# Kernel tuning notes

Hardware: AMD Instinct MI355X
Metric: run time of the kernel (lower is better)

## Reference

```python
import jax, jax.numpy as jnp
import numpy as np

B, NQ, C, H, P, DFF = 4, 2500, 256, 8, 8, 512
BEV_H, BEV_W = 200, 200
DH = C // H


def _ln(x, g, b, eps=1e-5):
    m = x.mean(-1, keepdims=True)
    v = ((x - m) ** 2).mean(-1, keepdims=True)
    return (x - m) / jnp.sqrt(v + eps) * g + b


def setup_inputs() -> dict:
    key = jax.random.key(0)
    ks = jax.random.split(key, 16)
    s = 0.02
    f32 = jnp.float32
    return {
        'query': jax.random.normal(ks[0], (B, NQ, C), f32),
        'value': jax.random.normal(ks[1], (B, BEV_H * BEV_W, C), f32),
        'query_pos': jax.random.normal(ks[2], (B, NQ, C), f32),
        'ref_2d': jax.random.uniform(ks[3], (B, NQ, 1, 2), f32),
        'in_proj_w': jax.random.normal(ks[4], (3 * C, C), f32) * s,
        'in_proj_b': jnp.zeros((3 * C,), f32),
        'out_proj_w': jax.random.normal(ks[5], (C, C), f32) * s,
        'out_proj_b': jnp.zeros((C,), f32),
        'off_w': jax.random.normal(ks[6], (H * P * 2, C), f32) * s,
        'off_b': jax.random.normal(ks[7], (H * P * 2,), f32),
        'aw_w': jax.random.normal(ks[8], (H * P, C), f32) * s,
        'aw_b': jnp.zeros((H * P,), f32),
        'vproj_w': jax.random.normal(ks[9], (C, C), f32) * s,
        'vproj_b': jnp.zeros((C,), f32),
        'oproj_w': jax.random.normal(ks[10], (C, C), f32) * s,
        'oproj_b': jnp.zeros((C,), f32),
        'ffn_w1': jax.random.normal(ks[11], (DFF, C), f32) * s,
        'ffn_b1': jnp.zeros((DFF,), f32),
        'ffn_w2': jax.random.normal(ks[12], (C, DFF), f32) * s,
        'ffn_b2': jnp.zeros((C,), f32),
        'ln1_g': jnp.ones((C,), f32), 'ln1_b': jnp.zeros((C,), f32),
        'ln2_g': jnp.ones((C,), f32), 'ln2_b': jnp.zeros((C,), f32),
        'ln3_g': jnp.ones((C,), f32), 'ln3_b': jnp.zeros((C,), f32),
        'bev_h': BEV_H,
        'bev_w': BEV_W,
    }


def _deform_attn(q, val_flat, ref, off_w, off_b, aw_w, aw_b,
                 vproj_w, vproj_b, oproj_w, oproj_b, bev_h, bev_w):
    # MSDeformAttn with n_levels=1 (Deformable-DETR math, align_corners=False bilinear).
    Bq, Nq, Cq = q.shape
    val = (val_flat @ vproj_w.T + vproj_b).reshape(Bq, bev_h * bev_w, H, DH)
    off = (q @ off_w.T + off_b).reshape(Bq, Nq, H, P, 2)
    aw = jax.nn.softmax((q @ aw_w.T + aw_b).reshape(Bq, Nq, H, P), axis=-1)
    norm = jnp.array([bev_w, bev_h], jnp.float32)  # offsets normalized by (W, H)
    # ref: (B, Nq, 1, 2) broadcasts over heads/points -> (B, Nq, H, P, 2)
    loc = ref[:, :, None, :, :] + off / norm
    # grid_sample(align_corners=False): pixel = loc * size - 0.5
    x = loc[..., 0] * bev_w - 0.5
    y = loc[..., 1] * bev_h - 0.5
    x0 = jnp.floor(x)
    y0 = jnp.floor(y)
    lx = x - x0
    ly = y - y0
    x0i = x0.astype(jnp.int32)
    y0i = y0.astype(jnp.int32)
    b_idx = jnp.arange(Bq)[:, None, None, None]
    h_idx = jnp.arange(H)[None, None, :, None]

    def gather(yi, xi):
        valid = (xi >= 0) & (xi < bev_w) & (yi >= 0) & (yi < bev_h)
        idx = jnp.clip(yi, 0, bev_h - 1) * bev_w + jnp.clip(xi, 0, bev_w - 1)
        g = val[b_idx, idx, h_idx]  # (B, Nq, H, P, DH)
        return g * valid[..., None]

    w00 = ((1 - lx) * (1 - ly))[..., None]
    w01 = (lx * (1 - ly))[..., None]
    w10 = ((1 - lx) * ly)[..., None]
    w11 = (lx * ly)[..., None]
    samp = (gather(y0i, x0i) * w00 + gather(y0i, x0i + 1) * w01
            + gather(y0i + 1, x0i) * w10 + gather(y0i + 1, x0i + 1) * w11)
    out = (samp * aw[..., None]).sum(axis=3).reshape(Bq, Nq, Cq)
    return out @ oproj_w.T + oproj_b


def _forward(query, value, query_pos, ref_2d,
             in_proj_w, in_proj_b, out_proj_w, out_proj_b,
             off_w, off_b, aw_w, aw_b, vproj_w, vproj_b, oproj_w, oproj_b,
             ffn_w1, ffn_b1, ffn_w2, ffn_b2,
             ln1_g, ln1_b, ln2_g, ln2_b, ln3_g, ln3_b, bev_h, bev_w):
    Bq, Nq, Cq = query.shape
    # ---- self attention (q = query + pos, k = v = query) ----
    Wq, Wk, Wv = in_proj_w[:C], in_proj_w[C:2 * C], in_proj_w[2 * C:]
    bq, bk, bv = in_proj_b[:C], in_proj_b[C:2 * C], in_proj_b[2 * C:]
    q = ((query + query_pos) @ Wq.T + bq).reshape(Bq, Nq, H, DH)
    k = (query @ Wk.T + bk).reshape(Bq, Nq, H, DH)
    v = (query @ Wv.T + bv).reshape(Bq, Nq, H, DH)
    scores = jnp.einsum('bqhd,bkhd->bhqk', q, k) / jnp.sqrt(jnp.float32(DH))
    attn = jax.nn.softmax(scores, axis=-1)
    sa = jnp.einsum('bhqk,bkhd->bqhd', attn, v).reshape(Bq, Nq, Cq)
    sa = sa @ out_proj_w.T + out_proj_b
    x = sa + query
    identity = x
    x = _ln(x, ln1_g, ln1_b)
    # ---- deformable cross attention ----
    ca = _deform_attn(x, value, ref_2d, off_w, off_b, aw_w, aw_b,
                      vproj_w, vproj_b, oproj_w, oproj_b, bev_h, bev_w)
    x = ca + identity
    x = _ln(x, ln2_g, ln2_b)
    # ---- FFN with internal residual ----
    x = x + (jax.nn.relu(x @ ffn_w1.T + ffn_b1) @ ffn_w2.T + ffn_b2)
    x = _ln(x, ln3_g, ln3_b)
    return x


def reference(query, value, query_pos, ref_2d,
              in_proj_w, in_proj_b, out_proj_w, out_proj_b,
              off_w, off_b, aw_w, aw_b, vproj_w, vproj_b, oproj_w, oproj_b,
              ffn_w1, ffn_b1, ffn_w2, ffn_b2,
              ln1_g, ln1_b, ln2_g, ln2_b, ln3_g, ln3_b, bev_h, bev_w):
    return _forward(query, value, query_pos, ref_2d,
                    in_proj_w, in_proj_b, out_proj_w, out_proj_b,
                    off_w, off_b, aw_w, aw_b, vproj_w, vproj_b, oproj_w, oproj_b,
                    ffn_w1, ffn_b1, ffn_w2, ffn_b2,
                    ln1_g, ln1_b, ln2_g, ln2_b, ln3_g, ln3_b, bev_h, bev_w)
```

## Files before the change

kernel.cpp:

```cpp
#include <hip/hip_runtime.h>

#define BB   4
#define NQ   2500
#define CC   256
#define HH   8
#define PP   8
#define DFFN 512
#define DH   32
#define BEV  200
#define NVAL (BEV * BEV)

typedef short bf16x8 __attribute__((ext_vector_type(8)));
typedef float f32x4  __attribute__((ext_vector_type(4)));

__device__ __forceinline__ unsigned short f2b(float f) {
    union { float f; unsigned int u; } v; v.f = f;
    unsigned int r = v.u + 0x7fffu + ((v.u >> 16) & 1u);
    return (unsigned short)(r >> 16);
}
__device__ __forceinline__ float b2f(unsigned short b) {
    union { unsigned int u; float f; } v; v.u = ((unsigned int)b) << 16;
    return v.f;
}

#define GLOAD16(g, l)                                                         \
    __builtin_amdgcn_global_load_lds(                                         \
        (const __attribute__((address_space(1))) void*)(g),                   \
        (__attribute__((address_space(3))) void*)(l), 16, 0, 0)

__global__ __launch_bounds__(256) void add_cvt_qp(const float* __restrict__ q,
                                                  const float* __restrict__ p,
                                                  unsigned short* __restrict__ qpb,
                                                  unsigned short* __restrict__ qb,
                                                  int n4) {
    int i = blockIdx.x * 256 + threadIdx.x;
    if (i < n4) {
        float4 a = reinterpret_cast<const float4*>(q)[i];
        float4 b = reinterpret_cast<const float4*>(p)[i];
        ushort4 s, t;
        s.x = f2b(a.x); s.y = f2b(a.y); s.z = f2b(a.z); s.w = f2b(a.w);
        t.x = f2b(a.x + b.x); t.y = f2b(a.y + b.y);
        t.z = f2b(a.z + b.z); t.w = f2b(a.w + b.w);
        reinterpret_cast<ushort4*>(qb)[i]  = s;
        reinterpret_cast<ushort4*>(qpb)[i] = t;
    }
}

__global__ __launch_bounds__(256) void cvt4(const float* __restrict__ in,
                                            unsigned short* __restrict__ out, int n4) {
    int i = blockIdx.x * 256 + threadIdx.x;
    if (i < n4) {
        float4 a = reinterpret_cast<const float4*>(in)[i];
        ushort4 s;
        s.x = f2b(a.x); s.y = f2b(a.y); s.z = f2b(a.z); s.w = f2b(a.w);
        reinterpret_cast<ushort4*>(out)[i] = s;
    }
}

__global__ __launch_bounds__(256) void cvt_weights(const float* __restrict__ in_w,
                                                   const float* __restrict__ outp_w,
                                                   const float* __restrict__ vproj_w,
                                                   const float* __restrict__ oproj_w,
                                                   const float* __restrict__ ffn_w1,
                                                   const float* __restrict__ ffn_w2,
                                                   unsigned short* __restrict__ Wb) {
    int i = blockIdx.x * 256 + threadIdx.x;
    if (i >= 163840) return;
    const float* src; int base;
    if      (i <  49152) { src = in_w;    base = 0;      }
    else if (i <  65536) { src = outp_w;  base = 49152;  }
    else if (i <  81920) { src = vproj_w; base = 65536;  }
    else if (i <  98304) { src = oproj_w; base = 81920;  }
    else if (i < 131072) { src = ffn_w1;  base = 98304;  }
    else                 { src = ffn_w2;  base = 131072; }
    float4 a = reinterpret_cast<const float4*>(src)[i - base];
    ushort4 s;
    s.x = f2b(a.x); s.y = f2b(a.y); s.z = f2b(a.z); s.w = f2b(a.w);
    reinterpret_cast<ushort4*>(Wb)[i] = s;
}

#define TM 128
#define TN 128
#define TK 32
template <bool RELU, bool OBF>
__global__ __launch_bounds__(256) void gemm_mfma(const unsigned short* __restrict__ A,
                                                 const unsigned short* __restrict__ W,
                                                 const float* __restrict__ bias,
                                                 float* __restrict__ Cf,
                                                 unsigned short* __restrict__ Cb,
                                                 int M, int N, int K) {
    __shared__ __align__(16) unsigned short As[TM * TK];
    __shared__ __align__(16) unsigned short Ws[TN * TK];
    const int t    = threadIdx.x;
    const int lane = t & 63;
    const int wv   = t >> 6;
    const int wr   = wv >> 1;
    const int wc   = wv & 1;
    const int m0 = blockIdx.y * TM;
    const int n0 = blockIdx.x * TN;
    const int l15 = lane & 15;
    const int l4  = lane >> 4;

    const int srow = (lane >> 2);
    const int skk  = (lane & 3) << 3;

    f32x4 acc[4][4];
#pragma unroll
    for (int i = 0; i < 4; i++)
#pragma unroll
        for (int j = 0; j < 4; j++) acc[i][j] = (f32x4){0.f, 0.f, 0.f, 0.f};

    for (int k0 = 0; k0 < K; k0 += TK) {
#pragma unroll
        for (int c2 = 0; c2 < 2; c2++) {
            const int c = wv * 2 + c2;
            const int row = c * 16 + srow;
            int ar = m0 + row; if (ar >= M) ar = M - 1;
            int br = n0 + row; if (br >= N) br = N - 1;
            GLOAD16(A + (size_t)ar * K + k0 + skk, As + c * 512);
            GLOAD16(W + (size_t)br * K + k0 + skk, Ws + c * 512);
        }
        __syncthreads();

        bf16x8 af[4], bfr[4];
#pragma unroll
        for (int i = 0; i < 4; i++) {
            af[i]  = *reinterpret_cast<const bf16x8*>(&As[(wr * 64 + i * 16 + l15) * TK + l4 * 8]);
            bfr[i] = *reinterpret_cast<const bf16x8*>(&Ws[(wc * 64 + i * 16 + l15) * TK + l4 * 8]);
        }
#pragma unroll
        for (int i = 0; i < 4; i++)
#pragma unroll
            for (int j = 0; j < 4; j++)
                acc[i][j] = __builtin_amdgcn_mfma_f32_16x16x32_bf16(af[i], bfr[j], acc[i][j], 0, 0, 0);
        __syncthreads();
    }

#pragma unroll
    for (int i = 0; i < 4; i++) {
#pragma unroll
        for (int j = 0; j < 4; j++) {
            const int col = n0 + wc * 64 + j * 16 + l15;
            const float bv = bias[col];
#pragma unroll
            for (int r = 0; r < 4; r++) {
                const int row = m0 + wr * 64 + i * 16 + l4 * 4 + r;
                if (row < M) {
                    float v = acc[i][j][r] + bv;
                    if (RELU) v = fmaxf(v, 0.f);
                    if (OBF) Cb[(size_t)row * N + col] = f2b(v);
                    else     Cf[(size_t)row * N + col] = v;
                }
            }
        }
    }
}

#define BM 64
#define BN 64
#define BK 16
__global__ __launch_bounds__(256) void gemm_bias(const float* __restrict__ A,
                                                 const float* __restrict__ W,
                                                 const float* __restrict__ bias,
                                                 float* __restrict__ C,
                                                 int M, int N, int K) {
    __shared__ float As[BK][BM + 4];
    __shared__ float Ws[BK][BN + 4];
    const int m0 = blockIdx.y * BM;
    const int n0 = blockIdx.x * BN;
    const int t  = threadIdx.x;
    const int tx = t & 15;
    const int ty = t >> 4;
    const int lrow = t >> 2;
    const int lk   = (t & 3) << 2;

    float acc[4][4];
#pragma unroll
    for (int i = 0; i < 4; i++)
#pragma unroll
        for (int j = 0; j < 4; j++) acc[i][j] = 0.f;

    const bool aok = (m0 + lrow) < M;
    const float* Ap = A + (size_t)(m0 + lrow) * K + lk;
    const float* Wp = W + (size_t)(n0 + lrow) * K + lk;

    for (int k0 = 0; k0 < K; k0 += BK) {
        float4 av = make_float4(0.f, 0.f, 0.f, 0.f);
        if (aok) av = *reinterpret_cast<const float4*>(Ap + k0);
        float4 wv = *reinterpret_cast<const float4*>(Wp + k0);
        As[lk + 0][lrow] = av.x; As[lk + 1][lrow] = av.y;
        As[lk + 2][lrow] = av.z; As[lk + 3][lrow] = av.w;
        Ws[lk + 0][lrow] = wv.x; Ws[lk + 1][lrow] = wv.y;
        Ws[lk + 2][lrow] = wv.z; Ws[lk + 3][lrow] = wv.w;
        __syncthreads();
#pragma unroll
        for (int kk = 0; kk < BK; kk++) {
            float4 a4 = *reinterpret_cast<const float4*>(&As[kk][ty << 2]);
            float4 w4 = *reinterpret_cast<const float4*>(&Ws[kk][tx << 2]);
            float a[4] = {a4.x, a4.y, a4.z, a4.w};
            float w[4] = {w4.x, w4.y, w4.z, w4.w};
#pragma unroll
            for (int i = 0; i < 4; i++)
#pragma unroll
                for (int j = 0; j < 4; j++)
                    acc[i][j] = fmaf(a[i], w[j], acc[i][j]);
        }
        __syncthreads();
    }

    float4 b4 = *reinterpret_cast<const float4*>(bias + n0 + (tx << 2));
#pragma unroll
    for (int i = 0; i < 4; i++) {
        int row = m0 + (ty << 2) + i;
        if (row < M) {
            float4 o;
            o.x = acc[i][0] + b4.x; o.y = acc[i][1] + b4.y;
            o.z = acc[i][2] + b4.z; o.w = acc[i][3] + b4.w;
            *reinterpret_cast<float4*>(C + (size_t)row * N + n0 + (tx << 2)) = o;
        }
    }
}

#define QT 64
#define KTT 64
#define NTQ ((NQ + QT - 1) / QT)
#define NTK ((NQ + KTT - 1) / KTT)
#define VLD (KTT + 8)

__global__ __launch_bounds__(256) void flash_mfma(const unsigned short* __restrict__ Q,
                                                  const unsigned short* __restrict__ K,
                                                  const unsigned short* __restrict__ V,
                                                  unsigned short* __restrict__ O) {
    __shared__ __align__(16) unsigned short VT[2][DH][VLD];
    __shared__ __align__(16) unsigned short PL[4][16][VLD];

    const int bh = blockIdx.y;
    const int b = bh >> 3, h = bh & 7;
    const int t = threadIdx.x;
    const int w = t >> 6;
    const int lane = t & 63;
    const int l15 = lane & 15;
    const int g = lane >> 4;
    const int q0 = blockIdx.x * QT;
    const float scale = 0.17677669529663687f;

    const size_t kvb = (size_t)b * NQ * CC + h * DH;

    int qr = q0 + w * 16 + l15; if (qr >= NQ) qr = NQ - 1;
    const bf16x8 qfrag = *reinterpret_cast<const bf16x8*>(Q + kvb + (size_t)qr * CC + g * 8);

    const int skey = t >> 2;
    const int sd0  = (t & 3) << 3;

    {
        int kr = skey; if (kr >= NQ) kr = NQ - 1;
        bf16x8 vv = *reinterpret_cast<const bf16x8*>(V + kvb + (size_t)kr * CC + sd0);
#pragma unroll
        for (int j2 = 0; j2 < 8; j2++) VT[0][sd0 + j2][skey] = (unsigned short)vv[j2];
    }
    bf16x8 kf[4];
#pragma unroll
    for (int j = 0; j < 4; j++) {
        int kr = j * 16 + l15; if (kr >= NQ) kr = NQ - 1;
        kf[j] = *reinterpret_cast<const bf16x8*>(K + kvb + (size_t)kr * CC + g * 8);
    }
    __syncthreads();

    float m = -1e30f, l = 0.f;
    f32x4 o0 = {0.f, 0.f, 0.f, 0.f}, o1 = {0.f, 0.f, 0.f, 0.f};

    for (int kt = 0; kt < NTK; kt++) {
        const int cur = kt & 1;

        if (kt + 1 < NTK) {
            int kr = (kt + 1) * KTT + skey; if (kr >= NQ) kr = NQ - 1;
            bf16x8 vv = *reinterpret_cast<const bf16x8*>(V + kvb + (size_t)kr * CC + sd0);
#pragma unroll
            for (int j2 = 0; j2 < 8; j2++) VT[cur ^ 1][sd0 + j2][skey] = (unsigned short)vv[j2];
        }

        f32x4 sf[4];
#pragma unroll
        for (int j = 0; j < 4; j++)
            sf[j] = __builtin_amdgcn_mfma_f32_16x16x32_bf16(kf[j], qfrag,
                                                            (f32x4){0.f, 0.f, 0.f, 0.f}, 0, 0, 0);

        if (kt + 1 < NTK) {
#pragma unroll
            for (int j = 0; j < 4; j++) {
                int kr = (kt + 1) * KTT + j * 16 + l15; if (kr >= NQ) kr = NQ - 1;
                kf[j] = *reinterpret_cast<const bf16x8*>(K + kvb + (size_t)kr * CC + g * 8);
            }
        }

        float sv[16];
#pragma unroll
        for (int j = 0; j < 4; j++)
#pragma unroll
            for (int r = 0; r < 4; r++) {
                int key = kt * KTT + j * 16 + g * 4 + r;
                sv[j * 4 + r] = (key < NQ) ? sf[j][r] * scale : -1e30f;
            }

        float mx = sv[0];
#pragma unroll
        for (int i = 1; i < 16; i++) mx = fmaxf(mx, sv[i]);
        mx = fmaxf(mx, __shfl_xor(mx, 16));
        mx = fmaxf(mx, __shfl_xor(mx, 32));
        float mn = fmaxf(m, mx);
        float cor = __expf(m - mn);
        m = mn;

        float ps = 0.f;
#pragma unroll
        for (int j = 0; j < 4; j++) {
            ushort4 pk;
            float p0 = __expf(sv[j * 4 + 0] - mn);
            float p1 = __expf(sv[j * 4 + 1] - mn);
            float p2 = __expf(sv[j * 4 + 2] - mn);
            float p3 = __expf(sv[j * 4 + 3] - mn);
            ps += (p0 + p1) + (p2 + p3);
            pk.x = f2b(p0); pk.y = f2b(p1); pk.z = f2b(p2); pk.w = f2b(p3);
            *reinterpret_cast<ushort4*>(&PL[w][l15][j * 16 + g * 4]) = pk;
        }
        ps += __shfl_xor(ps, 16);
        ps += __shfl_xor(ps, 32);
        l = l * cor + ps;
        o0 *= cor; o1 *= cor;

#pragma unroll
        for (int ks = 0; ks < 2; ks++) {
            bf16x8 pf = *reinterpret_cast<const bf16x8*>(&PL[w][l15][ks * 32 + g * 8]);
            bf16x8 va = *reinterpret_cast<const bf16x8*>(&VT[cur][l15][ks * 32 + g * 8]);
            bf16x8 vc = *reinterpret_cast<const bf16x8*>(&VT[cur][16 + l15][ks * 32 + g * 8]);
            o0 = __builtin_amdgcn_mfma_f32_16x16x32_bf16(va, pf, o0, 0, 0, 0);
            o1 = __builtin_amdgcn_mfma_f32_16x16x32_bf16(vc, pf, o1, 0, 0, 0);
        }

        __syncthreads();
    }

    int q = q0 + w * 16 + l15;
    if (q < NQ) {
        float inv = 1.f / l;
        unsigned short* op = O + ((size_t)b * NQ + q) * CC + h * DH;
#pragma unroll
        for (int r = 0; r < 4; r++) {
            op[g * 4 + r]      = f2b(o0[r] * inv);
            op[16 + g * 4 + r] = f2b(o1[r] * inv);
        }
    }
}

__global__ __launch_bounds__(256) void resid_ln(const float* __restrict__ a,
                                                const float* __restrict__ r,
                                                const float* __restrict__ g,
                                                const float* __restrict__ be,
                                                float* __restrict__ sum_out,
                                                float* __restrict__ ln_out,
                                                unsigned short* __restrict__ ln_bf) {
    const int row = blockIdx.x;
    const int t = threadIdx.x;
    const size_t base = (size_t)row * CC;
    float v = a[base + t] + r[base + t];
    if (sum_out) sum_out[base + t] = v;

    __shared__ float red[4];
    float s = v;
#pragma unroll
    for (int o = 1; o < 64; o <<= 1) s += __shfl_xor(s, o, 64);
    if ((t & 63) == 0) red[t >> 6] = s;
    __syncthreads();
    float mean = (red[0] + red[1] + red[2] + red[3]) * (1.f / 256.f);
    __syncthreads();

    float d = v - mean;
    float sq = d * d;
#pragma unroll
    for (int o = 1; o < 64; o <<= 1) sq += __shfl_xor(sq, o, 64);
    if ((t & 63) == 0) red[t >> 6] = sq;
    __syncthreads();
    float var = (red[0] + red[1] + red[2] + red[3]) * (1.f / 256.f);

    float res = d * rsqrtf(var + 1e-5f) * g[t] + be[t];
    ln_out[base + t] = res;
    if (ln_bf) ln_bf[base + t] = f2b(res);
}

__global__ __launch_bounds__(256) void deform_sample(const unsigned short* __restrict__ val,
                                                     const float* __restrict__ off,
                                                     const float* __restrict__ awl,
                                                     const float* __restrict__ ref,
                                                     unsigned short* __restrict__ out) {
    const int bq = blockIdx.x;
    const int b = bq / NQ;
    const int t = threadIdx.x;
    const int h = t >> 5, d = t & 31;

    const float rx = ref[(size_t)bq * 2 + 0];
    const float ry = ref[(size_t)bq * 2 + 1];

    const float* ap = awl + (size_t)bq * (HH * PP) + h * PP;
    float aw[PP];
    float mx = -1e30f;
#pragma unroll
    for (int p = 0; p < PP; p++) { aw[p] = ap[p]; mx = fmaxf(mx, aw[p]); }
    float se = 0.f;
#pragma unroll
    for (int p = 0; p < PP; p++) { aw[p] = __expf(aw[p] - mx); se += aw[p]; }
    const float inv = 1.f / se;

    const float* op = off + (size_t)bq * (HH * PP * 2) + h * (PP * 2);
    const unsigned short* vb = val + (size_t)b * NVAL * CC + h * DH + d;

    float acc = 0.f;
#pragma unroll
    for (int p = 0; p < PP; p++) {
        float x = (rx + op[p * 2 + 0] * (1.f / BEV)) * (float)BEV - 0.5f;
        float y = (ry + op[p * 2 + 1] * (1.f / BEV)) * (float)BEV - 0.5f;
        float xf = floorf(x), yf = floorf(y);
        float lx = x - xf, ly = y - yf;
        int x0 = (int)xf, y0 = (int)yf;
        float w = aw[p] * inv;

        float s = 0.f;
#pragma unroll
        for (int c = 0; c < 4; c++) {
            int xi = x0 + (c & 1);
            int yi = y0 + (c >> 1);
            float wx = (c & 1) ? lx : (1.f - lx);
            float wy = (c >> 1) ? ly : (1.f - ly);
            bool vld = (xi >= 0) && (xi < BEV) && (yi >= 0) && (yi < BEV);
            int xc = min(max(xi, 0), BEV - 1);
            int yc = min(max(yi, 0), BEV - 1);
            float gv = b2f(vb[(size_t)(yc * BEV + xc) * CC]);
            s += vld ? (wx * wy * gv) : 0.f;
        }
        acc = fmaf(w, s, acc);
    }
    out[(size_t)bq * CC + t] = f2b(acc);
}

extern "C" void kernel_launch(void* const* d_in, const int* in_sizes, int n_in,
                              void* d_out, int out_size, void* d_ws, size_t ws_size,
                              hipStream_t stream) {
    const float* query   = (const float*)d_in[0];
    const float* value   = (const float*)d_in[1];
    const float* qpos    = (const float*)d_in[2];
    const float* ref2d   = (const float*)d_in[3];
    const float* in_w    = (const float*)d_in[4];
    const float* in_b    = (const float*)d_in[5];
    const float* outp_w  = (const float*)d_in[6];
    const float* outp_b  = (const float*)d_in[7];
    const float* off_w   = (const float*)d_in[8];
    const float* off_b   = (const float*)d_in[9];
    const float* aw_w    = (const float*)d_in[10];
    const float* aw_b    = (const float*)d_in[11];
    const float* vproj_w = (const float*)d_in[12];
    const float* vproj_b = (const float*)d_in[13];
    const float* oproj_w = (const float*)d_in[14];
    const float* oproj_b = (const float*)d_in[15];
    const float* ffn_w1  = (const float*)d_in[16];
    const float* ffn_b1  = (const float*)d_in[17];
    const float* ffn_w2  = (const float*)d_in[18];
    const float* ffn_b2  = (const float*)d_in[19];
    const float* ln1_g = (const float*)d_in[20], *ln1_b = (const float*)d_in[21];
    const float* ln2_g = (const float*)d_in[22], *ln2_b = (const float*)d_in[23];
    const float* ln3_g = (const float*)d_in[24], *ln3_b = (const float*)d_in[25];

    float* ws = (float*)d_ws;
    float* out = (float*)d_out;

    const int M = BB * NQ;

    unsigned short* QPb    = (unsigned short*)ws;
    unsigned short* QUERYb = (unsigned short*)(ws + 1280000);
    unsigned short* Qbb    = (unsigned short*)(ws + 2560000);
    unsigned short* Kbb    = (unsigned short*)(ws + 3840000);
    unsigned short* Vbb    = (unsigned short*)(ws + 5120000);
    unsigned short* ATTb   = (unsigned short*)(ws + 6400000);
    float* SA   = ws + 7680000;
    unsigned short* VALUEb = (unsigned short*)ws;
    unsigned short* VALb = (unsigned short*)(ws + 20480000);
    float* B3   = ws + 40960000;
    float* X1   = B3;
    float* XLN1 = B3 + 2560000;
    float* OFF  = B3 + 5120000;
    float* AWL  = B3 + 6400000;
    unsigned short* SAMPb = (unsigned short*)(B3 + 7040000);
    float* CA   = B3 + 8320000;
    float* XLN2 = B3 + 10880000;
    unsigned short* XLN2b = (unsigned short*)(B3 + 13440000);
    unsigned short* FFNHb = (unsigned short*)(B3 + 14720000);
    float* FFNO = B3 + 17280000;
    unsigned short* Wb = (unsigned short*)(B3 + 19840000);

    dim3 blk(256);
    const int mgT = (M + TM - 1) / TM;

    add_cvt_qp<<<dim3(2500), blk, 0, stream>>>(query, qpos, QPb, QUERYb, 640000);
    cvt_weights<<<dim3(640), blk, 0, stream>>>(in_w, outp_w, vproj_w, oproj_w, ffn_w1, ffn_w2, Wb);
    gemm_mfma<false, true><<<dim3(2, mgT), blk, 0, stream>>>(QPb,    Wb,          in_b,        nullptr, Qbb, M, CC, CC);
    gemm_mfma<false, true><<<dim3(2, mgT), blk, 0, stream>>>(QUERYb, Wb + 65536,  in_b + CC,   nullptr, Kbb, M, CC, CC);
    gemm_mfma<false, true><<<dim3(2, mgT), blk, 0, stream>>>(QUERYb, Wb + 131072, in_b + 2*CC, nullptr, Vbb, M, CC, CC);
    flash_mfma<<<dim3(NTQ, BB * HH), blk, 0, stream>>>(Qbb, Kbb, Vbb, ATTb);
    gemm_mfma<false, false><<<dim3(2, mgT), blk, 0, stream>>>(ATTb, Wb + 196608, outp_b, SA, nullptr, M, CC, CC);
    resid_ln<<<dim3(M), blk, 0, stream>>>(SA, query, ln1_g, ln1_b, X1, XLN1, nullptr);
    gemm_bias<<<dim3(2, (M + BM - 1) / BM), blk, 0, stream>>>(XLN1, off_w, off_b, OFF, M, 128, CC);
    gemm_bias<<<dim3(1, (M + BM - 1) / BM), blk, 0, stream>>>(XLN1, aw_w,  aw_b,  AWL, M, 64,  CC);
    cvt4<<<dim3(40000), blk, 0, stream>>>(value, VALUEb, 10240000);
    gemm_mfma<false, true><<<dim3(2, (BB * NVAL) / TM), blk, 0, stream>>>(VALUEb, Wb + 262144, vproj_b, nullptr, VALb, BB * NVAL, CC, CC);
    deform_sample<<<dim3(M), blk, 0, stream>>>(VALb, OFF, AWL, ref2d, SAMPb);
    gemm_mfma<false, false><<<dim3(2, mgT), blk, 0, stream>>>(SAMPb, Wb + 327680, oproj_b, CA, nullptr, M, CC, CC);
    resid_ln<<<dim3(M), blk, 0, stream>>>(CA, X1, ln2_g, ln2_b, nullptr, XLN2, XLN2b);
    gemm_mfma<true,  true ><<<dim3(4, mgT), blk, 0, stream>>>(XLN2b, Wb + 393216, ffn_b1, nullptr, FFNHb, M, DFFN, CC);
    gemm_mfma<false, false><<<dim3(2, mgT), blk, 0, stream>>>(FFNHb, Wb + 524288, ffn_b2, FFNO, nullptr, M, CC, DFFN);
    resid_ln<<<dim3(M), blk, 0, stream>>>(FFNO, XLN2, ln3_g, ln3_b, nullptr, out, nullptr);
}
```

Baseline: 680.9 us.

## Fuse value conversion into vproj GEMM, split flash attention, merge K/V and off/aw GEMMs

Several independent changes land together. The separate fp32→bf16 conversion of the large value tensor is folded into a new vproj MFMA GEMM that converts while loading its A tile. The K and V projections become a single N=512 GEMM. Flash attention is split into two key chunks with a combine kernel, doubling grid parallelism. The fp32 SIMT offset and attention-weight GEMMs become one bf16 MFMA GEMM fed by a bf16 LN output. These remove a large intermediate round trip and some launches, at the cost of extra partial-result traffic for the attention split and bf16 rounding in the offset projection.

After: 639.0 us. -6.1%, faster.

```diff
diff --git a/kernel.cpp b/kernel.cpp
--- a/kernel.cpp
+++ b/kernel.cpp
@@ -11,6 +11,7 @@
 #define NVAL (BEV * BEV)
 
 typedef short bf16x8 __attribute__((ext_vector_type(8)));
+typedef unsigned short u16x8 __attribute__((ext_vector_type(8)));
 typedef float f32x4  __attribute__((ext_vector_type(4)));
 
 __device__ __forceinline__ unsigned short f2b(float f) {
@@ -46,33 +47,26 @@
     }
 }
 
-__global__ __launch_bounds__(256) void cvt4(const float* __restrict__ in,
-                                            unsigned short* __restrict__ out, int n4) {
-    int i = blockIdx.x * 256 + threadIdx.x;
-    if (i < n4) {
-        float4 a = reinterpret_cast<const float4*>(in)[i];
-        ushort4 s;
-        s.x = f2b(a.x); s.y = f2b(a.y); s.z = f2b(a.z); s.w = f2b(a.w);
-        reinterpret_cast<ushort4*>(out)[i] = s;
-    }
-}
-
 __global__ __launch_bounds__(256) void cvt_weights(const float* __restrict__ in_w,
                                                    const float* __restrict__ outp_w,
                                                    const float* __restrict__ vproj_w,
                                                    const float* __restrict__ oproj_w,
                                                    const float* __restrict__ ffn_w1,
                                                    const float* __restrict__ ffn_w2,
+                                                   const float* __restrict__ off_w,
+                                                   const float* __restrict__ aw_w,
                                                    unsigned short* __restrict__ Wb) {
     int i = blockIdx.x * 256 + threadIdx.x;
-    if (i >= 163840) return;
+    if (i >= 176128) return;
     const float* src; int base;
     if      (i <  49152) { src = in_w;    base = 0;      }
     else if (i <  65536) { src = outp_w;  base = 49152;  }
     else if (i <  81920) { src = vproj_w; base = 65536;  }
     else if (i <  98304) { src = oproj_w; base = 81920;  }
     else if (i < 131072) { src = ffn_w1;  base = 98304;  }
-    else                 { src = ffn_w2;  base = 131072; }
+    else if (i < 163840) { src = ffn_w2;  base = 131072; }
+    else if (i < 172032) { src = off_w;   base = 163840; }
+    else                 { src = aw_w;    base = 172032; }
     float4 a = reinterpret_cast<const float4*>(src)[i - base];
     ushort4 s;
     s.x = f2b(a.x); s.y = f2b(a.y); s.z = f2b(a.z); s.w = f2b(a.w);
@@ -156,67 +150,157 @@
     }
 }
 
-#define BM 64
-#define BN 64
-#define BK 16
-__global__ __launch_bounds__(256) void gemm_bias(const float* __restrict__ A,
-                                                 const float* __restrict__ W,
-                                                 const float* __restrict__ bias,
-                                                 float* __restrict__ C,
-                                                 int M, int N, int K) {
-    __shared__ float As[BK][BM + 4];
-    __shared__ float Ws[BK][BN + 4];
-    const int m0 = blockIdx.y * BM;
-    const int n0 = blockIdx.x * BN;
-    const int t  = threadIdx.x;
-    const int tx = t & 15;
-    const int ty = t >> 4;
-    const int lrow = t >> 2;
-    const int lk   = (t & 3) << 2;
-
-    float acc[4][4];
+#define VP_LDA 40
+__global__ __launch_bounds__(256) void gemm_vproj(const float* __restrict__ A,
+                                                  const unsigned short* __restrict__ W,
+                                                  const float* __restrict__ bias,
+                                                  unsigned short* __restrict__ Cb,
+                                                  int M, int N, int K) {
+    __shared__ __align__(16) unsigned short As[TM * VP_LDA];
+    __shared__ __align__(16) unsigned short Ws[TN * TK];
+    const int t    = threadIdx.x;
+    const int lane = t & 63;
+    const int wv   = t >> 6;
+    const int wr   = wv >> 1;
+    const int wc   = wv & 1;
+    const int m0 = blockIdx.y * TM;
+    const int n0 = blockIdx.x * TN;
+    const int l15 = lane & 15;
+    const int l4  = lane >> 4;
+    const int srow = (lane >> 2);
+    const int skk  = (lane & 3) << 3;
+    const int arow = t & 127;
+    const int akh  = t >> 7;
+
+    f32x4 acc[4][4];
 #pragma unroll
     for (int i = 0; i < 4; i++)
 #pragma unroll
-        for (int j = 0; j < 4; j++) acc[i][j] = 0.f;
-
-    const bool aok = (m0 + lrow) < M;
-    const float* Ap = A + (size_t)(m0 + lrow) * K + lk;
-    const float* Wp = W + (size_t)(n0 + lrow) * K + lk;
-
-    for (int k0 = 0; k0 < K; k0 += BK) {
-        float4 av = make_float4(0.f, 0.f, 0.f, 0.f);
-        if (aok) av = *reinterpret_cast<const float4*>(Ap + k0);
-        float4 wv = *reinterpret_cast<const float4*>(Wp + k0);
-        As[lk + 0][lrow] = av.x; As[lk + 1][lrow] = av.y;
-        As[lk + 2][lrow] = av.z; As[lk + 3][lrow] = av.w;
-        Ws[lk + 0][lrow] = wv.x; Ws[lk + 1][lrow] = wv.y;
-        Ws[lk + 2][lrow] = wv.z; Ws[lk + 3][lrow] = wv.w;
+        for (int j = 0; j < 4; j++) acc[i][j] = (f32x4){0.f, 0.f, 0.f, 0.f};
+
+    int ar = m0 + arow; if (ar >= M) ar = M - 1;
+    const float* ap = A + (size_t)ar * K + akh * 16;
+
+    for (int k0 = 0; k0 < K; k0 += TK) {
+#pragma unroll
+        for (int c2 = 0; c2 < 2; c2++) {
+            const int c = wv * 2 + c2;
+            int br = n0 + c * 16 + srow; if (br >= N) br = N - 1;
+            GLOAD16(W + (size_t)br * K + k0 + skk, Ws + c * 512);
+        }
+        float4 f0 = *reinterpret_cast<const float4*>(ap + k0);
+        float4 f1 = *reinterpret_cast<const float4*>(ap + k0 + 4);
+        float4 f2 = *reinterpret_cast<const float4*>(ap + k0 + 8);
+        float4 f3 = *reinterpret_cast<const float4*>(ap + k0 + 12);
+        u16x8 pa, pb;
+        pa[0] = f2b(f0.x); pa[1] = f2b(f0.y); pa[2] = f2b(f0.z); pa[3] = f2b(f0.w);
+        pa[4] = f2b(f1.x); pa[5] = f2b(f1.y); pa[6] = f2b(f1.z); pa[7] = f2b(f1.w);
+        pb[0] = f2b(f2.x); pb[1] = f2b(f2.y); pb[2] = f2b(f2.z); pb[3] = f2b(f2.w);
+        pb[4] = f2b(f3.x); pb[5] = f2b(f3.y); pb[6] = f2b(f3.z); pb[7] = f2b(f3.w);
+        *reinterpret_cast<u16x8*>(&As[arow * VP_LDA + akh * 16])     = pa;
+        *reinterpret_cast<u16x8*>(&As[arow * VP_LDA + akh * 16 + 8]) = pb;
         __syncthreads();
-#pragma unroll
-        for (int kk = 0; kk < BK; kk++) {
-            float4 a4 = *reinterpret_cast<const float4*>(&As[kk][ty << 2]);
-            float4 w4 = *reinterpret_cast<const float4*>(&Ws[kk][tx << 2]);
-            float a[4] = {a4.x, a4.y, a4.z, a4.w};
-            float w[4] = {w4.x, w4.y, w4.z, w4.w};
-#pragma unroll
-            for (int i = 0; i < 4; i++)
-#pragma unroll
-                for (int j = 0; j < 4; j++)
-                    acc[i][j] = fmaf(a[i], w[j], acc[i][j]);
-        }
+
+        bf16x8 af[4], bfr[4];
+#pragma unroll
+        for (int i = 0; i < 4; i++) {
+            af[i]  = *reinterpret_cast<const bf16x8*>(&As[(wr * 64 + i * 16 + l15) * VP_LDA + l4 * 8]);
+            bfr[i] = *reinterpret_cast<const bf16x8*>(&Ws[(wc * 64 + i * 16 + l15) * TK + l4 * 8]);
+        }
+#pragma unroll
+        for (int i = 0; i < 4; i++)
+#pragma unroll
+            for (int j = 0; j < 4; j++)
+                acc[i][j] = __builtin_amdgcn_mfma_f32_16x16x32_bf16(af[i], bfr[j], acc[i][j], 0, 0, 0);
         __syncthreads();
     }
 
-    float4 b4 = *reinterpret_cast<const float4*>(bias + n0 + (tx << 2));
 #pragma unroll
     for (int i = 0; i < 4; i++) {
-        int row = m0 + (ty << 2) + i;
-        if (row < M) {
-            float4 o;
-            o.x = acc[i][0] + b4.x; o.y = acc[i][1] + b4.y;
-            o.z = acc[i][2] + b4.z; o.w = acc[i][3] + b4.w;
-            *reinterpret_cast<float4*>(C + (size_t)row * N + n0 + (tx << 2)) = o;
+#pragma unroll
+        for (int j = 0; j < 4; j++) {
+            const int col = n0 + wc * 64 + j * 16 + l15;
+            const float bv = bias[col];
+#pragma unroll
+            for (int r = 0; r < 4; r++) {
+                const int row = m0 + wr * 64 + i * 16 + l4 * 4 + r;
+                if (row < M)
+                    Cb[(size_t)row * N + col] = f2b(acc[i][j][r] + bv);
+            }
+        }
+    }
+}
+
+__global__ __launch_bounds__(256) void gemm_offaw(const unsigned short* __restrict__ A,
+                                                  const unsigned short* __restrict__ W,
+                                                  const float* __restrict__ off_b,
+                                                  const float* __restrict__ aw_b,
+                                                  float* __restrict__ OFF,
+                                                  float* __restrict__ AWL,
+                                                  int M) {
+    __shared__ __align__(16) unsigned short As[TM * TK];
+    __shared__ __align__(16) unsigned short Ws[64 * TK];
+    const int t    = threadIdx.x;
+    const int lane = t & 63;
+    const int wv   = t >> 6;
+    const int wr   = wv >> 1;
+    const int wc   = wv & 1;
+    const int m0 = blockIdx.y * TM;
+    const int n0 = blockIdx.x * 64;
+    const int l15 = lane & 15;
+    const int l4  = lane >> 4;
+    const int srow = (lane >> 2);
+    const int skk  = (lane & 3) << 3;
+
+    f32x4 acc[4][2];
+#pragma unroll
+    for (int i = 0; i < 4; i++)
+#pragma unroll
+        for (int j = 0; j < 2; j++) acc[i][j] = (f32x4){0.f, 0.f, 0.f, 0.f};
+
+    for (int k0 = 0; k0 < 256; k0 += TK) {
+#pragma unroll
+        for (int c2 = 0; c2 < 2; c2++) {
+            const int c = wv * 2 + c2;
+            int ar = m0 + c * 16 + srow; if (ar >= M) ar = M - 1;
+            GLOAD16(A + (size_t)ar * 256 + k0 + skk, As + c * 512);
+        }
+        {
+            int br = n0 + wv * 16 + srow;
+            GLOAD16(W + (size_t)br * 256 + k0 + skk, Ws + wv * 512);
+        }
+        __syncthreads();
+
+        bf16x8 af[4], bw[2];
+#pragma unroll
+        for (int i = 0; i < 4; i++)
+            af[i] = *reinterpret_cast<const bf16x8*>(&As[(wr * 64 + i * 16 + l15) * TK + l4 * 8]);
+#pragma unroll
+        for (int j = 0; j < 2; j++)
+            bw[j] = *reinterpret_cast<const bf16x8*>(&Ws[(wc * 32 + j * 16 + l15) * TK + l4 * 8]);
+#pragma unroll
+        for (int i = 0; i < 4; i++)
+#pragma unroll
+            for (int j = 0; j < 2; j++)
+                acc[i][j] = __builtin_amdgcn_mfma_f32_16x16x32_bf16(af[i], bw[j], acc[i][j], 0, 0, 0);
+        __syncthreads();
+    }
+
+#pragma unroll
+    for (int i = 0; i < 4; i++) {
+#pragma unroll
+        for (int j = 0; j < 2; j++) {
+            const int gc = n0 + wc * 32 + j * 16 + l15;
+            const float bv = (gc < 128) ? off_b[gc] : aw_b[gc - 128];
+#pragma unroll
+            for (int r = 0; r < 4; r++) {
+                const int row = m0 + wr * 64 + i * 16 + l4 * 4 + r;
+                if (row < M) {
+                    float v = acc[i][j][r] + bv;
+                    if (gc < 128) OFF[(size_t)row * 128 + gc] = v;
+                    else          AWL[(size_t)row * 64 + (gc - 128)] = v;
+                }
+            }
         }
     }
 }
@@ -224,16 +308,18 @@
 #define QT 64
 #define KTT 64
 #define NTQ ((NQ + QT - 1) / QT)
-#define NTK ((NQ + KTT - 1) / KTT)
+#define CHK 1280
+#define NTK2 (CHK / KTT)
 #define VLD (KTT + 8)
 
-__global__ __launch_bounds__(256) void flash_mfma(const unsigned short* __restrict__ Q,
-                                                  const unsigned short* __restrict__ K,
-                                                  const unsigned short* __restrict__ V,
-                                                  unsigned short* __restrict__ O) {
+__global__ __launch_bounds__(256) void flash_part(const unsigned short* __restrict__ Q,
+                                                  const unsigned short* __restrict__ KV,
+                                                  float* __restrict__ PART,
+                                                  float* __restrict__ ML) {
     __shared__ __align__(16) unsigned short VT[2][DH][VLD];
     __shared__ __align__(16) unsigned short PL[4][16][VLD];
 
+    const int c  = blockIdx.z;
     const int bh = blockIdx.y;
     const int b = bh >> 3, h = bh & 7;
     const int t = threadIdx.x;
@@ -242,39 +328,40 @@
     const int l15 = lane & 15;
     const int g = lane >> 4;
     const int q0 = blockIdx.x * QT;
+    const int kc0 = c * CHK;
     const float scale = 0.17677669529663687f;
 
-    const size_t kvb = (size_t)b * NQ * CC + h * DH;
+    const size_t qbase = (size_t)b * NQ;
 
     int qr = q0 + w * 16 + l15; if (qr >= NQ) qr = NQ - 1;
-    const bf16x8 qfrag = *reinterpret_cast<const bf16x8*>(Q + kvb + (size_t)qr * CC + g * 8);
+    const bf16x8 qfrag = *reinterpret_cast<const bf16x8*>(Q + (qbase + qr) * CC + h * DH + g * 8);
 
     const int skey = t >> 2;
     const int sd0  = (t & 3) << 3;
 
     {
-        int kr = skey; if (kr >= NQ) kr = NQ - 1;
-        bf16x8 vv = *reinterpret_cast<const bf16x8*>(V + kvb + (size_t)kr * CC + sd0);
+        int kr = kc0 + skey; if (kr >= NQ) kr = NQ - 1;
+        bf16x8 vv = *reinterpret_cast<const bf16x8*>(KV + (qbase + kr) * 512 + 256 + h * DH + sd0);
 #pragma unroll
         for (int j2 = 0; j2 < 8; j2++) VT[0][sd0 + j2][skey] = (unsigned short)vv[j2];
     }
     bf16x8 kf[4];
 #pragma unroll
     for (int j = 0; j < 4; j++) {
-        int kr = j * 16 + l15; if (kr >= NQ) kr = NQ - 1;
-        kf[j] = *reinterpret_cast<const bf16x8*>(K + kvb + (size_t)kr * CC + g * 8);
+        int kr = kc0 + j * 16 + l15; if (kr >= NQ) kr = NQ - 1;
+        kf[j] = *reinterpret_cast<const bf16x8*>(KV + (qbase + kr) * 512 + h * DH + g * 8);
     }
     __syncthreads();
 
     float m = -1e30f, l = 0.f;
     f32x4 o0 = {0.f, 0.f, 0.f, 0.f}, o1 = {0.f, 0.f, 0.f, 0.f};
 
-    for (int kt = 0; kt < NTK; kt++) {
+    for (int kt = 0; kt < NTK2; kt++) {
         const int cur = kt & 1;
 
-        if (kt + 1 < NTK) {
-            int kr = (kt + 1) * KTT + skey; if (kr >= NQ) kr = NQ - 1;
-            bf16x8 vv = *reinterpret_cast<const bf16x8*>(V + kvb + (size_t)kr * CC + sd0);
+        if (kt + 1 < NTK2) {
+            int kr = kc0 + (kt + 1) * KTT + skey; if (kr >= NQ) kr = NQ - 1;
+            bf16x8 vv = *reinterpret_cast<const bf16x8*>(KV + (qbase + kr) * 512 + 256 + h * DH + sd0);
 #pragma unroll
             for (int j2 = 0; j2 < 8; j2++) VT[cur ^ 1][sd0 + j2][skey] = (unsigned short)vv[j2];
         }
@@ -285,11 +372,11 @@
             sf[j] = __builtin_amdgcn_mfma_f32_16x16x32_bf16(kf[j], qfrag,
                                                             (f32x4){0.f, 0.f, 0.f, 0.f}, 0, 0, 0);
 
-        if (kt + 1 < NTK) {
+        if (kt + 1 < NTK2) {
 #pragma unroll
             for (int j = 0; j < 4; j++) {
-                int kr = (kt + 1) * KTT + j * 16 + l15; if (kr >= NQ) kr = NQ - 1;
-                kf[j] = *reinterpret_cast<const bf16x8*>(K + kvb + (size_t)kr * CC + g * 8);
+                int kr = kc0 + (kt + 1) * KTT + j * 16 + l15; if (kr >= NQ) kr = NQ - 1;
+                kf[j] = *reinterpret_cast<const bf16x8*>(KV + (qbase + kr) * 512 + h * DH + g * 8);
             }
         }
 
@@ -298,7 +385,7 @@
         for (int j = 0; j < 4; j++)
 #pragma unroll
             for (int r = 0; r < 4; r++) {
-                int key = kt * KTT + j * 16 + g * 4 + r;
+                int key = kc0 + kt * KTT + j * 16 + g * 4 + r;
                 sv[j * 4 + r] = (key < NQ) ? sf[j][r] * scale : -1e30f;
             }
 
@@ -342,14 +429,36 @@
 
     int q = q0 + w * 16 + l15;
     if (q < NQ) {
-        float inv = 1.f / l;
-        unsigned short* op = O + ((size_t)b * NQ + q) * CC + h * DH;
-#pragma unroll
-        for (int r = 0; r < 4; r++) {
-            op[g * 4 + r]      = f2b(o0[r] * inv);
-            op[16 + g * 4 + r] = f2b(o1[r] * inv);
-        }
-    }
+        float* pp = PART + ((size_t)(c * (BB * HH) + bh) * NQ + q) * 32;
+        *reinterpret_cast<f32x4*>(pp + g * 4)      = o0;
+        *reinterpret_cast<f32x4*>(pp + 16 + g * 4) = o1;
+        if (g == 0) {
+            float* mp = ML + ((size_t)(c * (BB * HH) + bh) * NQ + q) * 2;
+            mp[0] = m; mp[1] = l;
+        }
+    }
+}
+
+__global__ __launch_bounds__(256) void flash_combine(const float* __restrict__ PART,
+                                                     const float* __restrict__ ML,
+                                                     unsigned short* __restrict__ O) {
+    const int idx = blockIdx.x * 256 + threadIdx.x;
+    const int bq = idx >> 8;
+    const int hd = idx & 255;
+    const int h = hd >> 5, dd = hd & 31;
+    const int b = bq / NQ, q = bq - b * NQ;
+    const int bh = b * HH + h;
+
+    const float* mp0 = ML + ((size_t)bh * NQ + q) * 2;
+    const float* mp1 = ML + ((size_t)(32 + bh) * NQ + q) * 2;
+    float m0 = mp0[0], l0 = mp0[1];
+    float m1 = mp1[0], l1 = mp1[1];
+    float M = fmaxf(m0, m1);
+    float w0 = __expf(m0 - M), w1 = __expf(m1 - M);
+    float L = w0 * l0 + w1 * l1;
+    float S = w0 * PART[((size_t)bh * NQ + q) * 32 + dd]
+            + w1 * PART[((size_t)(32 + bh) * NQ + q) * 32 + dd];
+    O[idx] = f2b(S / L);
 }
 
 __global__ __launch_bounds__(256) void resid_ln(const float* __restrict__ a,
@@ -383,8 +492,8 @@
     float var = (red[0] + red[1] + red[2] + red[3]) * (1.f / 256.f);
 
     float res = d * rsqrtf(var + 1e-5f) * g[t] + be[t];
-    ln_out[base + t] = res;
-    if (ln_bf) ln_bf[base + t] = f2b(res);
+    if (ln_out) ln_out[base + t] = res;
+    if (ln_bf)  ln_bf[base + t] = f2b(res);
 }
 
 __global__ __launch_bounds__(256) void deform_sample(const unsigned short* __restrict__ val,
@@ -476,40 +585,39 @@
     unsigned short* QPb    = (unsigned short*)ws;
     unsigned short* QUERYb = (unsigned short*)(ws + 1280000);
     unsigned short* Qbb    = (unsigned short*)(ws + 2560000);
-    unsigned short* Kbb    = (unsigned short*)(ws + 3840000);
-    unsigned short* Vbb    = (unsigned short*)(ws + 5120000);
+    unsigned short* KVb    = (unsigned short*)(ws + 3840000);
     unsigned short* ATTb   = (unsigned short*)(ws + 6400000);
     float* SA   = ws + 7680000;
-    unsigned short* VALUEb = (unsigned short*)ws;
+    float* PART = ws + 10240000;
+    float* ML   = ws + 15360000;
     unsigned short* VALb = (unsigned short*)(ws + 20480000);
     float* B3   = ws + 40960000;
     float* X1   = B3;
-    float* XLN1 = B3 + 2560000;
-    float* OFF  = B3 + 5120000;
-    float* AWL  = B3 + 6400000;
-    unsigned short* SAMPb = (unsigned short*)(B3 + 7040000);
-    float* CA   = B3 + 8320000;
-    float* XLN2 = B3 + 10880000;
-    unsigned short* XLN2b = (unsigned short*)(B3 + 13440000);
-    unsigned short* FFNHb = (unsigned short*)(B3 + 14720000);
-    float* FFNO = B3 + 17280000;
-    unsigned short* Wb = (unsigned short*)(B3 + 19840000);
+    unsigned short* XLN1b = (unsigned short*)(B3 + 2560000);
+    float* OFF  = B3 + 3840000;
+    float* AWL  = B3 + 5120000;
+    unsigned short* SAMPb = (unsigned short*)(B3 + 5760000);
+    float* CA   = B3 + 7040000;
+    float* XLN2 = B3 + 9600000;
+    unsigned short* XLN2b = (unsigned short*)(B3 + 12160000);
+    unsigned short* FFNHb = (unsigned short*)(B3 + 13440000);
+    float* FFNO = B3 + 16000000;
+    unsigned short* Wb = (unsigned short*)(B3 + 18560000);
 
     dim3 blk(256);
     const int mgT = (M + TM - 1) / TM;
 
     add_cvt_qp<<<dim3(2500), blk, 0, stream>>>(query, qpos, QPb, QUERYb, 640000);
-    cvt_weights<<<dim3(640), blk, 0, stream>>>(in_w, outp_w, vproj_w, oproj_w, ffn_w1, ffn_w2, Wb);
-    gemm_mfma<false, true><<<dim3(2, mgT), blk, 0, stream>>>(QPb,    Wb,          in_b,        nullptr, Qbb, M, CC, CC);
-    gemm_mfma<false, true><<<dim3(2, mgT), blk, 0, stream>>>(QUERYb, Wb + 65536,  in_b + CC,   nullptr, Kbb, M, CC, CC);
-    gemm_mfma<false, true><<<dim3(2, mgT), blk, 0, stream>>>(QUERYb, Wb + 131072, in_b + 2*CC, nullptr, Vbb, M, CC, CC);
-    flash_mfma<<<dim3(NTQ, BB * HH), blk, 0, stream>>>(Qbb, Kbb, Vbb, ATTb);
+    cvt_weights<<<dim3(688), blk, 0, stream>>>(in_w, outp_w, vproj_w, oproj_w,
+                                               ffn_w1, ffn_w2, off_w, aw_w, Wb);
+    gemm_mfma<false, true><<<dim3(2, mgT), blk, 0, stream>>>(QPb,    Wb,         in_b,       nullptr, Qbb, M, CC, CC);
+    gemm_mfma<false, true><<<dim3(4, mgT), blk, 0, stream>>>(QUERYb, Wb + 65536, in_b + CC,  nullptr, KVb, M, 512, CC);
+    flash_part<<<dim3(NTQ, BB * HH, 2), blk, 0, stream>>>(Qbb, KVb, PART, ML);
+    flash_combine<<<dim3(M), blk, 0, stream>>>(PART, ML, ATTb);
     gemm_mfma<false, false><<<dim3(2, mgT), blk, 0, stream>>>(ATTb, Wb + 196608, outp_b, SA, nullptr, M, CC, CC);
-    resid_ln<<<dim3(M), blk, 0, stream>>>(SA, query, ln1_g, ln1_b, X1, XLN1, nullptr);
-    gemm_bias<<<dim3(2, (M + BM - 1) / BM), blk, 0, stream>>>(XLN1, off_w, off_b, OFF, M, 128, CC);
-    gemm_bias<<<dim3(1, (M + BM - 1) / BM), blk, 0, stream>>>(XLN1, aw_w,  aw_b,  AWL, M, 64,  CC);
-    cvt4<<<dim3(40000), blk, 0, stream>>>(value, VALUEb, 10240000);
-    gemm_mfma<false, true><<<dim3(2, (BB * NVAL) / TM), blk, 0, stream>>>(VALUEb, Wb + 262144, vproj_b, nullptr, VALb, BB * NVAL, CC, CC);
+    resid_ln<<<dim3(M), blk, 0, stream>>>(SA, query, ln1_g, ln1_b, X1, nullptr, XLN1b);
+    gemm_offaw<<<dim3(3, mgT), blk, 0, stream>>>(XLN1b, Wb + 655360, off_b, aw_b, OFF, AWL, M);
+    gemm_vproj<<<dim3(2, (BB * NVAL) / TM), blk, 0, stream>>>(value, Wb + 262144, vproj_b, VALb, BB * NVAL, CC, CC);
     deform_sample<<<dim3(M), blk, 0, stream>>>(VALb, OFF, AWL, ref2d, SAMPb);
     gemm_mfma<false, false><<<dim3(2, mgT), blk, 0, stream>>>(SAMPb, Wb + 327680, oproj_b, CA, nullptr, M, CC, CC);
     resid_ln<<<dim3(M), blk, 0, stream>>>(CA, X1, ln2_g, ln2_b, nullptr, XLN2, XLN2b);
```
